# Performance work log

Hardware: AMD Instinct MI355X
Metric: run time of the kernel (lower is better)

The kernel has to match this reference:

```python
import jax, jax.numpy as jnp
import numpy as np

N, E = 25000, 400000
HID, EDGE_F, DIM, HEADS, ADY = 128, 16, 3, 8, 64
INNER = int(1.25 * HID)          # 160
MSG_F = 2 * HID + EDGE_F + 1     # 273 (e3, relaxed=False -> 1 distance feature)


def silu(x):
    return x * jax.nn.sigmoid(x)


def ada_ln(x, y, W, b):
    # LayerNorm (no affine) + FiLM conditioning from y
    mu = jnp.mean(x, axis=-1, keepdims=True)
    var = jnp.var(x, axis=-1, keepdims=True)
    xn = (x - mu) * jax.lax.rsqrt(var + 1e-5)
    scale, shift = jnp.split(y @ W + b, 2, axis=-1)
    return xn * (1.0 + scale) + shift


def setup_inputs() -> dict:
    key = jax.random.key(0)
    ks = jax.random.split(key, 32)
    rn = lambda k, shp, s=0.05: (jax.random.normal(k, shp, jnp.float32) * s)
    inp = {
        'h': jax.random.normal(ks[0], (N, HID), jnp.float32),
        'coords': jax.random.normal(ks[1], (N, DIM), jnp.float32),
        'a': jax.random.normal(ks[2], (E, EDGE_F), jnp.float32),
        'y': jax.random.normal(ks[3], (N, ADY), jnp.float32),
        'res': jnp.zeros((N, HID), jnp.float32),
        'src': jax.random.randint(ks[4], (E,), 0, N, jnp.int32),
        'dst': jax.random.randint(ks[5], (E,), 0, N, jnp.int32),
        # edge MLP
        'We1': rn(ks[6], (MSG_F, INNER)), 'be1': jnp.zeros((INNER,), jnp.float32),
        'We2': rn(ks[7], (INNER, INNER)), 'be2': jnp.zeros((INNER,), jnp.float32),
        # coord head (xavier gain 0.001 -> tiny init)
        'Wc': rn(ks[8], (INNER, 1), 0.001),
        # attention/value/output heads
        'Wv': rn(ks[9], (INNER, HID)),
        'Wa': rn(ks[10], (INNER, HEADS)),
        'Wo': rn(ks[11], (HID, HID)),
        # node MLP
        'Wn1': rn(ks[12], (HID, INNER)), 'bn1': jnp.zeros((INNER,), jnp.float32),
        'Wn2': rn(ks[13], (INNER, HID)), 'bn2': jnp.zeros((HID,), jnp.float32),
        # adaptive LayerNorms (FiLM from y)
        'Wf1': rn(ks[14], (ADY, 2 * HID)), 'bf1': jnp.zeros((2 * HID,), jnp.float32),
        'Wf2': rn(ks[15], (ADY, 2 * HID)), 'bf2': jnp.zeros((2 * HID,), jnp.float32),
    }
    return inp


def reference(h, coords, a, y, res, src, dst,
              We1, be1, We2, be2, Wc, Wv, Wa, Wo,
              Wn1, bn1, Wn2, bn2, Wf1, bf1, Wf2, bf2):
    n = h.shape[0]
    heads = Wa.shape[1]
    # --- distance features (e3, relaxed=False): radial only ---
    xs, xd = coords[src], coords[dst]          # [E, 3]
    diffs = xs - xd
    radials = jnp.sum(diffs * diffs, axis=-1, keepdims=True)  # [E, 1]
    # --- edge MLP on gathered features ---
    f = jnp.concatenate([h[src], h[dst], radials, a], axis=-1)  # [E, 273]
    m = silu(f @ We1 + be1)
    m = silu(m @ We2 + be2)                    # [E, inner]
    # --- coordinate messages + scatter-sum to dst ---
    msg_x = (m @ Wc) * diffs / (jnp.sqrt(radials + 1e-5) + 1.0)  # [E, 3]
    coords_out = coords + jax.ops.segment_sum(msg_x, dst, num_segments=n)
    # --- edge softmax over incoming edges per dst node ---
    logits = m @ Wa                             # [E, heads]
    mx = jax.ops.segment_max(logits, dst, num_segments=n)
    ex = jnp.exp(logits - mx[dst])
    den = jax.ops.segment_sum(ex, dst, num_segments=n)
    w = ex / den[dst]                           # [E, heads]
    # --- weighted value aggregation ---
    vals = (m @ Wv).reshape(-1, heads, HID // heads) * w[:, :, None]
    h_agg = jax.ops.segment_sum(vals, dst, num_segments=n).reshape(n, HID)
    f2 = h_agg @ Wo
    res1 = res + f2
    h1 = ada_ln(h + f2, y, Wf1, bf1)
    f3 = silu(h1 @ Wn1 + bn1) @ Wn2 + bn2
    res2 = res1 + f3
    h2 = ada_ln(h1 + f3, y, Wf2, bf2)
    return (h2, coords_out, res2)
```

## Files before the change

### kernel.cpp

```cpp
#include <hip/hip_runtime.h>
#include <math.h>

#define N_NODES 25000
#define N_EDGES 400000
#define HID 128
#define EDGE_F 16
#define ADY 64
#define INNER 160
#define MSG_F 273
#define HEADS 8

#define OUT_CRD (N_NODES * HID)
#define OUT_RES (N_NODES * (HID + 3))

#define FLAG_OFF 0
#define DEN_OFF  256
#define CACC_OFF 800256
#define HAGG_OFF 1100256
#define CNT_OFF  13900256
#define CUR_OFF  14000256
#define PERM_OFF 14100256
#define MEMSET_BYTES 14000256
#define HBF_OFF  15700256
#define YBF_OFF  22100256
#define BIAS_OFF 25300256
#define BW_OFF   25302560

#define SCR_STRIDE 145

typedef unsigned short u16;
typedef unsigned int u32;
typedef unsigned long long u64;
typedef __attribute__((ext_vector_type(8))) short short8;
typedef __attribute__((ext_vector_type(4))) float f32x4;

__device__ __forceinline__ float bf2f(u16 v) {
    union { u32 u; float f; } x; x.u = ((u32)v) << 16; return x.f;
}
__device__ __forceinline__ u16 f2bf(float f) {
    union { float ff; u32 u; } x; x.ff = f;
    u32 u = x.u;
    u32 rounding = 0x7FFFu + ((u >> 16) & 1u);
    u += rounding;
    return (u16)(u >> 16);
}
__device__ __forceinline__ float silu(float z) {
    z = fminf(fmaxf(z, -30000.f), 30000.f);
    return z / (1.0f + __expf(-z));
}

template<bool F32> __device__ __forceinline__ float ldg1(const void* p, size_t i) {
    if (F32) return ((const float*)p)[i];
    return bf2f(((const u16*)p)[i]);
}
template<bool F32> __device__ __forceinline__ void stg1(void* p, size_t i, float v) {
    if (F32) ((float*)p)[i] = v;
    else     ((u16*)p)[i] = f2bf(v);
}
__device__ __forceinline__ float ldany(const void* p, size_t i, bool f32) {
    return f32 ? ((const float*)p)[i] : bf2f(((const u16*)p)[i]);
}
__device__ __forceinline__ void wave_lds_fence() {
    __builtin_amdgcn_wave_barrier();
    __builtin_amdgcn_s_waitcnt(0xc07f);
    __builtin_amdgcn_wave_barrier();
}

struct CvtArgs {
    const void* src[8];
    u64 dstoff[8];
    int n[8];
};
struct BwArgs {
    const void* We1; const void* We2; const void* Wv; const void* Wa;
    const void* Wc;  const void* Wo;  const void* Wn1; const void* Wn2;
    const void* Wf1; const void* Wf2;
    u64 b1, b2, b3, b4, b5, b6, b7, b8;
};

__global__ __launch_bounds__(256)
void preproc_kernel(const void* hsrc, int* flag, char* ws, CvtArgs args, BwArgs bwa,
                    const int* __restrict__ dstp, int* __restrict__ cnt)
{
    __shared__ float red[256];
    __shared__ int sflag;
    const int t = threadIdx.x;
    {
        const u16* p = (const u16*)hsrc;
        float mx = 0.f;
        for (int i = 0; i < 8; i++) {
            int idx = (t * 8 + i) * 97;
            float v = fabsf(bf2f(p[idx * 2]));
            mx = fmaxf(mx, v);
        }
        red[t] = mx;
        __syncthreads();
        for (int s = 128; s > 0; s >>= 1) {
            if (t < s) red[t] = fmaxf(red[t], red[t + s]);
            __syncthreads();
        }
        if (t == 0) {
            sflag = (red[0] > 1e10f || red[0] == 0.f) ? 1 : 0;
            if (blockIdx.x == 0) flag[0] = sflag;
        }
        __syncthreads();
    }
    const bool f32 = (sflag != 0);
    const int g = blockIdx.x * 256 + t;
    const int stride = gridDim.x * 256;

    for (int i = g; i < N_EDGES; i += stride)
        atomicAdd(&cnt[dstp[i]], 1);

    for (int ten = 0; ten < 8; ten++) {
        const void* s = args.src[ten];
        u16* d = (u16*)(ws + args.dstoff[ten]);
        const int n = args.n[ten];
        if (f32) {
            const float* sf = (const float*)s;
            for (int i = g; i < n; i += stride) d[i] = f2bf(sf[i]);
        } else {
            const u16* su = (const u16*)s;
            for (int i = g; i < n; i += stride) d[i] = su[i];
        }
    }

    u16* b1 = (u16*)(ws + bwa.b1);
    u16* b2 = (u16*)(ws + bwa.b2);
    u16* b3 = (u16*)(ws + bwa.b3);
    u16* b4 = (u16*)(ws + bwa.b4);
    u16* b5 = (u16*)(ws + bwa.b5);
    u16* b6 = (u16*)(ws + bwa.b6);
    u16* b7 = (u16*)(ws + bwa.b7);
    u16* b8 = (u16*)(ws + bwa.b8);
    for (int i = g; i < 5*2*10*512; i += stride) {
        int tt = i >> 9, r = i & 511, l = r >> 3, j = r & 7;
        int c = tt / 20, ks = (tt / 10) % 2, nt = tt % 10;
        int k = c*64 + ks*32 + (l >> 4)*8 + j;
        int n = nt*16 + (l & 15);
        float v = 0.f;
        if (k < MSG_F)      v = ldany(bwa.We1, (size_t)k*INNER + n, f32);
        else if (k == 273)  v = ldany(bwa.We1, (size_t)256*INNER + n, f32);
        b1[i] = f2bf(v);
    }
    for (int i = g; i < 5*10*512; i += stride) {
        int tt = i >> 9, r = i & 511, l = r >> 3, j = r & 7;
        int k5 = tt / 10, nt = tt % 10;
        int k = k5*32 + (l >> 4)*8 + j;
        int n = nt*16 + (l & 15);
        b2[i] = f2bf(ldany(bwa.We2, (size_t)k*INNER + n, f32));
    }
    for (int i = g; i < 5*9*512; i += stride) {
        int tt = i >> 9, r = i & 511, l = r >> 3, j = r & 7;
        int k5 = tt / 9, nt = tt % 9;
        int k = k5*32 + (l >> 4)*8 + j;
        int n = nt*16 + (l & 15);
        float v = 0.f;
        if (n < 128)       v = ldany(bwa.Wv, (size_t)k*HID + n, f32);
        else if (n < 136)  v = ldany(bwa.Wa, (size_t)k*HEADS + (n-128), f32);
        else if (n == 136) v = ldany(bwa.Wc, (size_t)k, f32);
        b3[i] = f2bf(v);
    }
    for (int i = g; i < 4*8*512; i += stride) {
        int tt = i >> 9, r = i & 511, l = r >> 3, j = r & 7;
        int cks = tt / 8, nt = tt % 8;
        int k = cks*32 + (l >> 4)*8 + j;
        int n = nt*16 + (l & 15);
        b4[i] = f2bf(ldany(bwa.Wo, (size_t)k*HID + n, f32));
    }
    for (int i = g; i < 4*10*512; i += stride) {
        int tt = i >> 9, r = i & 511, l = r >> 3, j = r & 7;
        int cks = tt / 10, nt = tt % 10;
        int k = cks*32 + (l >> 4)*8 + j;
        int n = nt*16 + (l & 15);
        b5[i] = f2bf(ldany(bwa.Wn1, (size_t)k*INNER + n, f32));
    }
    for (int i = g; i < 5*8*512; i += stride) {
        int tt = i >> 9, r = i & 511, l = r >> 3, j = r & 7;
        int k5 = tt / 8, nt = tt % 8;
        int k = k5*32 + (l >> 4)*8 + j;
        int n = nt*16 + (l & 15);
        b6[i] = f2bf(ldany(bwa.Wn2, (size_t)k*HID + n, f32));
    }
    for (int i = g; i < 2*16*512; i += stride) {
        int tt = i >> 9, r = i & 511, l = r >> 3, j = r & 7;
        int ks = tt / 16, nt = tt % 16;
        int k = ks*32 + (l >> 4)*8 + j;
        int n = nt*16 + (l & 15);
        b7[i] = f2bf(ldany(bwa.Wf1, (size_t)k*256 + n, f32));
        b8[i] = f2bf(ldany(bwa.Wf2, (size_t)k*256 + n, f32));
    }
}

__global__ __launch_bounds__(1024)
void scan_kernel(const int* __restrict__ cnt, int* __restrict__ cursor)
{
    __shared__ int ssum[1024];
    const int t = threadIdx.x;
    const int base = t * 25;
    int loc[25];
    int s = 0;
    #pragma unroll
    for (int j = 0; j < 25; j++) {
        int i = base + j;
        int v = (i < N_NODES) ? cnt[i] : 0;
        loc[j] = s; s += v;
    }
    ssum[t] = s;
    __syncthreads();
    for (int off = 1; off < 1024; off <<= 1) {
        int v = (t >= off) ? ssum[t - off] : 0;
        __syncthreads();
        ssum[t] += v;
        __syncthreads();
    }
    int offs = (t > 0) ? ssum[t - 1] : 0;
    #pragma unroll
    for (int j = 0; j < 25; j++) {
        int i = base + j;
        if (i < N_NODES) cursor[i] = offs + loc[j];
    }
}

__global__ __launch_bounds__(256)
void scatter_kernel(const int* __restrict__ dstp, int* __restrict__ cursor,
                    int* __restrict__ perm)
{
    int i = blockIdx.x * 256 + threadIdx.x;
    if (i < N_EDGES) {
        int pos = atomicAdd(&cursor[dstp[i]], 1);
        perm[pos] = i;
    }
}

template<bool F32>
__device__ __forceinline__ void edge_body(
    const u16* __restrict__ hbf, const void* coords, const void* a,
    const int* __restrict__ src, const int* __restrict__ dst,
    const int* __restrict__ perm,
    const u16* __restrict__ We1P, const u16* __restrict__ We2P,
    const u16* __restrict__ W3P,
    const u16* __restrict__ cbe1, const u16* __restrict__ cbe2,
    float* __restrict__ den, float* __restrict__ hagg, float* __restrict__ cacc,
    u16* sPool, float* sdiff, float* srad, int* ssrc, int* sdstl, int* sedge)
{
    const int t   = threadIdx.x;
    const int w   = t >> 6;
    const int l   = t & 63;
    const int col = l & 15;
    const int q   = l >> 4;
    const int e0  = blockIdx.x * 64;
    const int l8  = l << 3;

    u16* sF  = sPool;
    u16* sM1 = sPool;
    u16* sM2 = sPool + 64*168;

    if (t < 64) {
        int e = perm[e0 + t];
        sedge[t] = e;
        int s = src[e], d = dst[e];
        ssrc[t] = s; sdstl[t] = d;
        float dx = ldg1<F32>(coords, (size_t)s*3+0) - ldg1<F32>(coords, (size_t)d*3+0);
        float dy = ldg1<F32>(coords, (size_t)s*3+1) - ldg1<F32>(coords, (size_t)d*3+1);
        float dz = ldg1<F32>(coords, (size_t)s*3+2) - ldg1<F32>(coords, (size_t)d*3+2);
        sdiff[t*4+0] = dx; sdiff[t*4+1] = dy; sdiff[t*4+2] = dz;
        float r2 = dx*dx + dy*dy + dz*dz;
        srad[t] = r2;
        sdiff[t*4+3] = 1.0f / (sqrtf(r2 + 1e-5f) + 1.0f);
    }
    __syncthreads();

    {
        int e = t >> 2, part = t & 3;
        int node_s = ssrc[e], node_d = sdstl[e];
        int ge = sedge[e];
        #pragma unroll
        for (int c = 0; c < 4; c++) {
            int node = (c < 2) ? node_s : node_d;
            int c0 = (c & 1) * 64 + part * 16;
            const uint4* gp = (const uint4*)(hbf + (size_t)node*HID + c0);
            *(uint4*)(&sF[e*360 + c*72 + part*16])     = gp[0];
            *(uint4*)(&sF[e*360 + c*72 + part*16 + 8]) = gp[1];
        }
        if (part < 2) {
            __align__(16) u16 tmp[16];
            #pragma unroll
            for (int j = 0; j < 16; j++) tmp[j] = 0;
            if (part == 0) {
                float r2 = srad[e];
                tmp[0] = f2bf(r2);
                for (int j = 0; j < 15; j++)
                    tmp[1+j] = f2bf(ldg1<F32>(a, (size_t)ge*EDGE_F + j));
            } else {
                tmp[0] = f2bf(ldg1<F32>(a, (size_t)ge*EDGE_F + 15));
                float r2 = srad[e];
                tmp[1] = f2bf(r2 - bf2f(f2bf(r2)));
            }
            *(uint4*)(&sF[e*360 + 4*72 + part*16])     = ((uint4*)tmp)[0];
            *(uint4*)(&sF[e*360 + 4*72 + part*16 + 8]) = ((uint4*)tmp)[1];
        }
    }
    __syncthreads();

    f32x4 acc1[10];
    #pragma unroll
    for (int nt = 0; nt < 10; nt++) {
        float v = bf2f(cbe1[nt*16 + col]);
        acc1[nt] = (f32x4){v, v, v, v};
    }
    const u16* fbase = &sF[(w*16 + col)*360];
    #pragma unroll
    for (int c = 0; c < 4; c++) {
        #pragma unroll
        for (int ks = 0; ks < 2; ks++) {
            short8 af = *(const short8*)(fbase + c*72 + ks*32 + q*8);
            const u16* B1 = We1P + (((c*2 + ks)*10) << 9) + l8;
            #pragma unroll
            for (int nt = 0; nt < 10; nt++) {
                short8 b = *(const short8*)(B1 + (nt << 9));
                acc1[nt] = __builtin_amdgcn_mfma_f32_16x16x32_bf16(af, b, acc1[nt], 0, 0, 0);
            }
        }
    }
    {
        short8 af = *(const short8*)(fbase + 4*72 + q*8);
        const u16* B1 = We1P + ((8*10) << 9) + l8;
        #pragma unroll
        for (int nt = 0; nt < 10; nt++) {
            short8 b = *(const short8*)(B1 + (nt << 9));
            acc1[nt] = __builtin_amdgcn_mfma_f32_16x16x32_bf16(af, b, acc1[nt], 0, 0, 0);
        }
    }
    __syncthreads();
    #pragma unroll
    for (int nt = 0; nt < 10; nt++)
        #pragma unroll
        for (int r = 0; r < 4; r++)
            sM1[(w*16 + q*4 + r)*168 + nt*16 + col] = f2bf(silu(acc1[nt][r]));
    __syncthreads();

    f32x4 acc2[10];
    #pragma unroll
    for (int nt = 0; nt < 10; nt++) {
        float v = bf2f(cbe2[nt*16 + col]);
        acc2[nt] = (f32x4){v, v, v, v};
    }
    const u16* m1base = &sM1[(w*16 + col)*168];
    #pragma unroll
    for (int k5 = 0; k5 < 5; k5++) {
        short8 af = *(const short8*)(m1base + k5*32 + q*8);
        const u16* B2 = We2P + ((k5*10) << 9) + l8;
        #pragma unroll
        for (int nt = 0; nt < 10; nt++) {
            short8 b = *(const short8*)(B2 + (nt << 9));
            acc2[nt] = __builtin_amdgcn_mfma_f32_16x16x32_bf16(af, b, acc2[nt], 0, 0, 0);
        }
    }
    #pragma unroll
    for (int nt = 0; nt < 10; nt++)
        #pragma unroll
        for (int r = 0; r < 4; r++)
            sM2[(w*16 + q*4 + r)*168 + nt*16 + col] = f2bf(silu(acc2[nt][r]));
    __syncthreads();

    f32x4 acc3[9];
    #pragma unroll
    for (int nt = 0; nt < 9; nt++) acc3[nt] = (f32x4){0.f, 0.f, 0.f, 0.f};
    const u16* m2base = &sM2[(w*16 + col)*168];
    #pragma unroll
    for (int k5 = 0; k5 < 5; k5++) {
        short8 af = *(const short8*)(m2base + k5*32 + q*8);
        const u16* B3 = W3P + ((k5*9) << 9) + l8;
        #pragma unroll
        for (int nt = 0; nt < 9; nt++) {
            short8 b = *(const short8*)(B3 + (nt << 9));
            acc3[nt] = __builtin_amdgcn_mfma_f32_16x16x32_bf16(af, b, acc3[nt], 0, 0, 0);
        }
    }
    __syncthreads();

    float* scr = (float*)(void*)sPool + (size_t)w * 16 * SCR_STRIDE;

    {
        float exv[4] = {0.f, 0.f, 0.f, 0.f};
        if (col < 8) {
            #pragma unroll
            for (int r = 0; r < 4; r++)
                exv[r] = __expf(fminf(fmaxf(acc3[8][r], -30.f), 30.f));
        }
        #pragma unroll
        for (int nt = 0; nt < 8; nt++) {
            float ex0 = __shfl(exv[0], q*16 + nt);
            float ex1 = __shfl(exv[1], q*16 + nt);
            float ex2 = __shfl(exv[2], q*16 + nt);
            float ex3 = __shfl(exv[3], q*16 + nt);
            scr[(q*4 + 0)*SCR_STRIDE + nt*16 + col] = acc3[nt][0] * ex0;
            scr[(q*4 + 1)*SCR_STRIDE + nt*16 + col] = acc3[nt][1] * ex1;
            scr[(q*4 + 2)*SCR_STRIDE + nt*16 + col] = acc3[nt][2] * ex2;
            scr[(q*4 + 3)*SCR_STRIDE + nt*16 + col] = acc3[nt][3] * ex3;
        }
        if (col < 8) {
            #pragma unroll
            for (int r = 0; r < 4; r++)
                scr[(q*4 + r)*SCR_STRIDE + 128 + col] = exv[r];
        }
        if (col == 8) {
            #pragma unroll
            for (int r = 0; r < 4; r++) {
                int idx = w*16 + q*4 + r;
                float invf = sdiff[idx*4 + 3];
                float lc = fminf(fmaxf(acc3[8][r], -1e6f), 1e6f) * invf;
                #pragma unroll
                for (int j = 0; j < 3; j++)
                    scr[(q*4 + r)*SCR_STRIDE + 136 + j] = lc * sdiff[idx*4 + j];
            }
        }
    }
    wave_lds_fence();

    {
        const int rbase = w*16;
        int dsts[16];
        #pragma unroll
        for (int row = 0; row < 16; row++) dsts[row] = sdstl[rbase + row];

        #pragma unroll
        for (int pass = 0; pass < 3; pass++) {
            int c = pass*64 + l;
            bool act = c < 139;
            float accu = 0.f;
            int prevd = dsts[0];
            #pragma unroll
            for (int row = 0; row < 16; row++) {
                int d = dsts[row];
                if (d != prevd) {
                    if (act) {
                        if (c < 128)      atomicAdd(&hagg[(size_t)prevd*HID + c], accu);
                        else if (c < 136) atomicAdd(&den[(size_t)prevd*8 + (c-128)], accu);
                        else              atomicAdd(&cacc[(size_t)prevd*3 + (c-136)], accu);
                    }
                    accu = 0.f; prevd = d;
                }
                if (act) accu += scr[row*SCR_STRIDE + c];
            }
            if (act) {
                if (c < 128)      atomicAdd(&hagg[(size_t)prevd*HID + c], accu);
                else if (c < 136) atomicAdd(&den[(size_t)prevd*8 + (c-128)], accu);
                else              atomicAdd(&cacc[(size_t)prevd*3 + (c-136)], accu);
            }
        }
    }
}

__global__ __launch_bounds__(256, 3)
void edge_kernel(const int* __restrict__ flag,
                 const u16* __restrict__ hbf, const void* coords, const void* a,
                 const int* __restrict__ src, const int* __restrict__ dst,
                 const int* __restrict__ perm,
                 const u16* __restrict__ We1P, const u16* __restrict__ We2P,
                 const u16* __restrict__ W3P,
                 const u16* __restrict__ cbe1, const u16* __restrict__ cbe2,
                 float* __restrict__ den, float* __restrict__ hagg,
                 float* __restrict__ cacc)
{
    __shared__ __align__(16) u16 sPool[64*360];
    __shared__ float sdiff[64*4];
    __shared__ float srad[64];
    __shared__ int   ssrc[64];
    __shared__ int   sdstl[64];
    __shared__ int   sedge[64];
    if (*flag)
        edge_body<true>(hbf, coords, a, src, dst, perm, We1P, We2P, W3P, cbe1, cbe2,
                        den, hagg, cacc, sPool, sdiff, srad, ssrc, sdstl, sedge);
    else
        edge_body<false>(hbf, coords, a, src, dst, perm, We1P, We2P, W3P, cbe1, cbe2,
                         den, hagg, cacc, sPool, sdiff, srad, ssrc, sdstl, sedge);
}

template<bool F32>
__device__ __forceinline__ void node_body(
    const u16* __restrict__ hbf, const void* res, const void* coords,
    const u16* __restrict__ ybf,
    const float* __restrict__ den, const float* __restrict__ hagg,
    const float* __restrict__ cacc,
    const u16* __restrict__ WoP, const u16* __restrict__ Wn1P,
    const u16* __restrict__ Wn2P, const u16* __restrict__ Wf1P,
    const u16* __restrict__ Wf2P,
    const u16* __restrict__ cbn1, const u16* __restrict__ cbn2,
    const u16* __restrict__ cbf1, const u16* __restrict__ cbf2,
    void* out, u16* sScr)
{
    const int t = threadIdx.x;
    const int w = t >> 6, l = t & 63, col = l & 15, q = l >> 4;
    const int nodew = blockIdx.x * 64 + w * 16;
    const int mynode = nodew + col;
    const bool okA = mynode < N_NODES;
    const int l8 = l << 3;
    u16* sc = sScr + w * 16 * 168;

    int gm[4]; bool okC[4];
    #pragma unroll
    for (int r = 0; r < 4; r++) { gm[r] = nodew + q*4 + r; okC[r] = gm[r] < N_NODES; }

    f32x4 aF2[8];
    #pragma unroll
    for (int nt = 0; nt < 8; nt++) aF2[nt] = (f32x4){0.f,0.f,0.f,0.f};
    #pragma unroll
    for (int c = 0; c < 2; c++) {
        #pragma unroll
        for (int ks = 0; ks < 2; ks++) {
            const int kbase = c*64 + ks*32 + q*8;
            union { u16 s[8]; short8 v; } u;
            if (okA) {
                float dd = den[(size_t)mynode*8 + (kbase >> 4)];
                float inv = dd > 0.f ? 1.f/dd : 0.f;
                const float4* gp = (const float4*)(hagg + (size_t)mynode*HID + kbase);
                float4 v0 = gp[0], v1 = gp[1];
                u.s[0]=f2bf(v0.x*inv); u.s[1]=f2bf(v0.y*inv); u.s[2]=f2bf(v0.z*inv); u.s[3]=f2bf(v0.w*inv);
                u.s[4]=f2bf(v1.x*inv); u.s[5]=f2bf(v1.y*inv); u.s[6]=f2bf(v1.z*inv); u.s[7]=f2bf(v1.w*inv);
            } else {
                #pragma unroll
                for (int j = 0; j < 8; j++) u.s[j] = 0;
            }
            const u16* B = WoP + (((c*2 + ks)*8) << 9) + l8;
            #pragma unroll
            for (int nt = 0; nt < 8; nt++) {
                short8 b = *(const short8*)(B + (nt << 9));
                aF2[nt] = __builtin_amdgcn_mfma_f32_16x16x32_bf16(u.v, b, aF2[nt], 0, 0, 0);
            }
        }
    }

    f32x4 aFl[16];
    #pragma unroll
    for (int nt = 0; nt < 16; nt++) {
        float v = bf2f(cbf1[nt*16 + col]);
        aFl[nt] = (f32x4){v,v,v,v};
    }
    #pragma unroll
    for (int ks = 0; ks < 2; ks++) {
        short8 af;
        if (okA) af = *(const short8*)(ybf + (size_t)mynode*ADY + ks*32 + q*8);
        else { union { u16 s[8]; short8 v; } z; for (int j=0;j<8;j++) z.s[j]=0; af = z.v; }
        const u16* B = Wf1P + ((ks*16) << 9) + l8;
        #pragma unroll
        for (int nt = 0; nt < 16; nt++) {
            short8 b = *(const short8*)(B + (nt << 9));
            aFl[nt] = __builtin_amdgcn_mfma_f32_16x16x32_bf16(af, b, aFl[nt], 0, 0, 0);
        }
    }

    float h1c[8][4], r1c[8][4];
    {
        float xv[8][4], s[4], ss[4];
        #pragma unroll
        for (int r = 0; r < 4; r++) { s[r] = 0.f; ss[r] = 0.f; }
        #pragma unroll
        for (int nt = 0; nt < 8; nt++)
            #pragma unroll
            for (int r = 0; r < 4; r++) {
                float hv = okC[r] ? bf2f(hbf[(size_t)gm[r]*HID + nt*16 + col]) : 0.f;
                float x = hv + aF2[nt][r];
                xv[nt][r] = x; s[r] += x; ss[r] += x*x;
            }
        #pragma unroll
        for (int r = 0; r < 4; r++)
            for (int off = 1; off <= 8; off <<= 1) {
                s[r]  += __shfl_xor(s[r], off);
                ss[r] += __shfl_xor(ss[r], off);
            }
        #pragma unroll
        for (int r = 0; r < 4; r++) {
            float mu = s[r] * (1.f/128.f);
            float var = ss[r] * (1.f/128.f) - mu*mu;
            float rs = rsqrtf(fmaxf(var, 0.f) + 1e-5f);
            #pragma unroll
            for (int nt = 0; nt < 8; nt++) {
                float h1 = (xv[nt][r]-mu)*rs*(1.f+aFl[nt][r]) + aFl[nt+8][r];
                h1c[nt][r] = h1;
                float rv = okC[r] ? ldg1<F32>(res, (size_t)gm[r]*HID + nt*16 + col) : 0.f;
                r1c[nt][r] = rv + aF2[nt][r];
                sc[(q*4 + r)*168 + nt*16 + col] = f2bf(h1);
            }
        }
    }
    wave_lds_fence();

    f32x4 aT[10];
    #pragma unroll
    for (int nt = 0; nt < 10; nt++) {
        float v = bf2f(cbn1[nt*16 + col]);
        aT[nt] = (f32x4){v,v,v,v};
    }
    #pragma unroll
    for (int c = 0; c < 2; c++) {
        #pragma unroll
        for (int ks = 0; ks < 2; ks++) {
            short8 af = *(const short8*)(sc + col*168 + c*64 + ks*32 + q*8);
            const u16* B = Wn1P + (((c*2 + ks)*10) << 9) + l8;
            #pragma unroll
            for (int nt = 0; nt < 10; nt++) {
                short8 b = *(const short8*)(B + (nt << 9));
                aT[nt] = __builtin_amdgcn_mfma_f32_16x16x32_bf16(af, b, aT[nt], 0, 0, 0);
            }
        }
    }
    wave_lds_fence();
    #pragma unroll
    for (int nt = 0; nt < 10; nt++)
        #pragma unroll
        for (int r = 0; r < 4; r++)
            sc[(q*4 + r)*168 + nt*16 + col] = f2bf(silu(aT[nt][r]));
    wave_lds_fence();

    f32x4 aF3[8];
    #pragma unroll
    for (int nt = 0; nt < 8; nt++) {
        float v = bf2f(cbn2[nt*16 + col]);
        aF3[nt] = (f32x4){v,v,v,v};
    }
    #pragma unroll
    for (int k5 = 0; k5 < 5; k5++) {
        short8 af = *(const short8*)(sc + col*168 + k5*32 + q*8);
        const u16* B = Wn2P + ((k5*8) << 9) + l8;
        #pragma unroll
        for (int nt = 0; nt < 8; nt++) {
            short8 b = *(const short8*)(B + (nt << 9));
            aF3[nt] = __builtin_amdgcn_mfma_f32_16x16x32_bf16(af, b, aF3[nt], 0, 0, 0);
        }
    }

    #pragma unroll
    for (int nt = 0; nt < 16; nt++) {
        float v = bf2f(cbf2[nt*16 + col]);
        aFl[nt] = (f32x4){v,v,v,v};
    }
    #pragma unroll
    for (int ks = 0; ks < 2; ks++) {
        short8 af;
        if (okA) af = *(const short8*)(ybf + (size_t)mynode*ADY + ks*32 + q*8);
        else { union { u16 s[8]; short8 v; } z; for (int j=0;j<8;j++) z.s[j]=0; af = z.v; }
        const u16* B = Wf2P + ((ks*16) << 9) + l8;
        #pragma unroll
        for (int nt = 0; nt < 16; nt++) {
            short8 b = *(const short8*)(B + (nt << 9));
            aFl[nt] = __builtin_amdgcn_mfma_f32_16x16x32_bf16(af, b, aFl[nt], 0, 0, 0);
        }
    }

    {
        float xv[8][4], s[4], ss[4];
        #pragma unroll
        for (int r = 0; r < 4; r++) { s[r] = 0.f; ss[r] = 0.f; }
        #pragma unroll
        for (int nt = 0; nt < 8; nt++)
            #pragma unroll
            for (int r = 0; r < 4; r++) {
                float x = h1c[nt][r] + aF3[nt][r];
                xv[nt][r] = x; s[r] += x; ss[r] += x*x;
            }
        #pragma unroll
        for (int r = 0; r < 4; r++)
            for (int off = 1; off <= 8; off <<= 1) {
                s[r]  += __shfl_xor(s[r], off);
                ss[r] += __shfl_xor(ss[r], off);
            }
        #pragma unroll
        for (int r = 0; r < 4; r++) {
            float mu = s[r] * (1.f/128.f);
            float var = ss[r] * (1.f/128.f) - mu*mu;
            float rs = rsqrtf(fmaxf(var, 0.f) + 1e-5f);
            if (okC[r]) {
                #pragma unroll
                for (int nt = 0; nt < 8; nt++) {
                    int n = nt*16 + col;
                    float h2 = (xv[nt][r]-mu)*rs*(1.f+aFl[nt][r]) + aFl[nt+8][r];
                    stg1<F32>(out, (size_t)gm[r]*HID + n, h2);
                    stg1<F32>(out, (size_t)OUT_RES + (size_t)gm[r]*HID + n,
                              r1c[nt][r] + aF3[nt][r]);
                }
            }
        }
    }

    if (q == 0 && okA) {
        #pragma unroll
        for (int j = 0; j < 3; j++)
            stg1<F32>(out, (size_t)OUT_CRD + (size_t)mynode*3 + j,
                      ldg1<F32>(coords, (size_t)mynode*3 + j) + cacc[(size_t)mynode*3 + j]);
    }
}

__global__ __launch_bounds__(256, 2)
void node_kernel(const int* __restrict__ flag,
                 const u16* __restrict__ hbf, const void* res, const void* coords,
                 const u16* __restrict__ ybf,
                 const float* __restrict__ den, const float* __restrict__ hagg,
                 const float* __restrict__ cacc,
                 const u16* __restrict__ WoP, const u16* __restrict__ Wn1P,
                 const u16* __restrict__ Wn2P, const u16* __restrict__ Wf1P,
                 const u16* __restrict__ Wf2P,
                 const u16* __restrict__ cbn1, const u16* __restrict__ cbn2,
                 const u16* __restrict__ cbf1, const u16* __restrict__ cbf2,
                 void* out)
{
    __shared__ __align__(16) u16 sScr[4 * 16 * 168];
    if (*flag)
        node_body<true>(hbf, res, coords, ybf, den, hagg, cacc, WoP, Wn1P, Wn2P,
                        Wf1P, Wf2P, cbn1, cbn2, cbf1, cbf2, out, sScr);
    else
        node_body<false>(hbf, res, coords, ybf, den, hagg, cacc, WoP, Wn1P, Wn2P,
                         Wf1P, Wf2P, cbn1, cbn2, cbf1, cbf2, out, sScr);
}

extern "C" void kernel_launch(void* const* d_in, const int* in_sizes, int n_in,
                              void* d_out, int out_size, void* d_ws, size_t ws_size,
                              hipStream_t stream)
{
    const void* h      = d_in[0];
    const void* coords = d_in[1];
    const void* a      = d_in[2];
    const void* y      = d_in[3];
    const void* res    = d_in[4];
    const int* src     = (const int*)d_in[5];
    const int* dst     = (const int*)d_in[6];

    char* ws = (char*)d_ws;
    int*   flag   = (int*)(ws + FLAG_OFF);
    float* den    = (float*)(ws + DEN_OFF);
    float* cacc   = (float*)(ws + CACC_OFF);
    float* hagg   = (float*)(ws + HAGG_OFF);
    int*   cnt    = (int*)(ws + CNT_OFF);
    int*   cursor = (int*)(ws + CUR_OFF);
    int*   perm   = (int*)(ws + PERM_OFF);
    u16*   hbf    = (u16*)(ws + HBF_OFF);
    u16*   ybf    = (u16*)(ws + YBF_OFF);

    CvtArgs args;
    const int cvtn[8]   = {160, 160, 160, 128, 256, 256, N_NODES*HID, N_NODES*ADY};
    const int cvtsrc[8] = {8, 10, 16, 18, 20, 22, 0, 3};
    u64 boff[8];
    u64 bo = BIAS_OFF;
    for (int i = 0; i < 6; i++) {
        boff[i] = bo;
        bo += ((u64)cvtn[i] * 2 + 15) & ~(u64)15;
    }
    boff[6] = HBF_OFF;
    boff[7] = YBF_OFF;
    for (int i = 0; i < 8; i++) {
        args.src[i] = d_in[cvtsrc[i]];
        args.dstoff[i] = boff[i];
        args.n[i] = cvtn[i];
    }
    const u16* cbe1 = (const u16*)(ws + boff[0]);
    const u16* cbe2 = (const u16*)(ws + boff[1]);
    const u16* cbn1 = (const u16*)(ws + boff[2]);
    const u16* cbn2 = (const u16*)(ws + boff[3]);
    const u16* cbf1 = (const u16*)(ws + boff[4]);
    const u16* cbf2 = (const u16*)(ws + boff[5]);

    BwArgs bwa;
    bwa.We1 = d_in[7];  bwa.We2 = d_in[9];  bwa.Wv = d_in[12]; bwa.Wa = d_in[13];
    bwa.Wc  = d_in[11]; bwa.Wo  = d_in[14]; bwa.Wn1 = d_in[15]; bwa.Wn2 = d_in[17];
    bwa.Wf1 = d_in[19]; bwa.Wf2 = d_in[21];
    bwa.b1 = BW_OFF;
    bwa.b2 = bwa.b1 + (u64)5*2*10*512*2;
    bwa.b3 = bwa.b2 + (u64)5*10*512*2;
    bwa.b4 = bwa.b3 + (u64)5*9*512*2;
    bwa.b5 = bwa.b4 + (u64)4*8*512*2;
    bwa.b6 = bwa.b5 + (u64)4*10*512*2;
    bwa.b7 = bwa.b6 + (u64)5*8*512*2;
    bwa.b8 = bwa.b7 + (u64)2*16*512*2;
    const u16* We1P = (const u16*)(ws + bwa.b1);
    const u16* We2P = (const u16*)(ws + bwa.b2);
    const u16* W3P  = (const u16*)(ws + bwa.b3);
    const u16* WoP  = (const u16*)(ws + bwa.b4);
    const u16* Wn1P = (const u16*)(ws + bwa.b5);
    const u16* Wn2P = (const u16*)(ws + bwa.b6);
    const u16* Wf1P = (const u16*)(ws + bwa.b7);
    const u16* Wf2P = (const u16*)(ws + bwa.b8);

    hipMemsetAsync(d_ws, 0, MEMSET_BYTES, stream);

    preproc_kernel<<<256, 256, 0, stream>>>(h, flag, ws, args, bwa, dst, cnt);

    scan_kernel<<<1, 1024, 0, stream>>>(cnt, cursor);

    scatter_kernel<<<(N_EDGES + 255)/256, 256, 0, stream>>>(dst, cursor, perm);

    edge_kernel<<<N_EDGES/64, 256, 0, stream>>>(flag, hbf, coords, a, src, dst, perm,
                                                We1P, We2P, W3P, cbe1, cbe2,
                                                den, hagg, cacc);

    node_kernel<<<(N_NODES + 63)/64, 256, 0, stream>>>(
        flag, hbf, res, coords, ybf, den, hagg, cacc,
        WoP, Wn1P, Wn2P, Wf1P, Wf2P, cbn1, cbn2, cbf1, cbf2, d_out);
}
```

Before: 528.0 us.

## Make edge kernel wave-private in LDS with MFMA-fragment layout, drop block barriers

Each wave now gathers its own 16 edges into a private LDS slice stored directly in the MFMA A-fragment layout. This replaces the block-wide staging and the __syncthreads calls with wave-local fences, and per-edge geometry is passed through shuffles instead of shared arrays. The shared memory footprint shrinks, so launch bounds are raised to 4 blocks per CU for more occupancy. The costs are a higher register-pressure ceiling and redundant index loads across the 4 lanes per edge.

Result: faster. 482.1 us (-8.7%).

```diff
diff --git a/kernel.cpp b/kernel.cpp
--- a/kernel.cpp
+++ b/kernel.cpp
@@ -26,6 +26,7 @@
 #define BIAS_OFF 25300256
 #define BW_OFF   25302560
 
+#define WSLICE 5120
 #define SCR_STRIDE 145
 
 typedef unsigned short u16;
@@ -64,6 +65,10 @@
     __builtin_amdgcn_wave_barrier();
     __builtin_amdgcn_s_waitcnt(0xc07f);
     __builtin_amdgcn_wave_barrier();
+}
+
+__device__ __forceinline__ int a_addr(int k, int lr) {
+    return ((k >> 5) << 9) + (((((k & 31) >> 3) << 4) | lr) << 3) + (k & 7);
 }
 
 struct CvtArgs {
@@ -242,7 +247,7 @@
     const u16* __restrict__ W3P,
     const u16* __restrict__ cbe1, const u16* __restrict__ cbe2,
     float* __restrict__ den, float* __restrict__ hagg, float* __restrict__ cacc,
-    u16* sPool, float* sdiff, float* srad, int* ssrc, int* sdstl, int* sedge)
+    u16* sPool)
 {
     const int t   = threadIdx.x;
     const int w   = t >> 6;
@@ -252,56 +257,47 @@
     const int e0  = blockIdx.x * 64;
     const int l8  = l << 3;
 
-    u16* sF  = sPool;
-    u16* sM1 = sPool;
-    u16* sM2 = sPool + 64*168;
-
-    if (t < 64) {
-        int e = perm[e0 + t];
-        sedge[t] = e;
-        int s = src[e], d = dst[e];
-        ssrc[t] = s; sdstl[t] = d;
-        float dx = ldg1<F32>(coords, (size_t)s*3+0) - ldg1<F32>(coords, (size_t)d*3+0);
-        float dy = ldg1<F32>(coords, (size_t)s*3+1) - ldg1<F32>(coords, (size_t)d*3+1);
-        float dz = ldg1<F32>(coords, (size_t)s*3+2) - ldg1<F32>(coords, (size_t)d*3+2);
-        sdiff[t*4+0] = dx; sdiff[t*4+1] = dy; sdiff[t*4+2] = dz;
-        float r2 = dx*dx + dy*dy + dz*dz;
-        srad[t] = r2;
-        sdiff[t*4+3] = 1.0f / (sqrtf(r2 + 1e-5f) + 1.0f);
-    }
-    __syncthreads();
-
-    {
-        int e = t >> 2, part = t & 3;
-        int node_s = ssrc[e], node_d = sdstl[e];
-        int ge = sedge[e];
-        #pragma unroll
-        for (int c = 0; c < 4; c++) {
-            int node = (c < 2) ? node_s : node_d;
-            int c0 = (c & 1) * 64 + part * 16;
-            const uint4* gp = (const uint4*)(hbf + (size_t)node*HID + c0);
-            *(uint4*)(&sF[e*360 + c*72 + part*16])     = gp[0];
-            *(uint4*)(&sF[e*360 + c*72 + part*16 + 8]) = gp[1];
-        }
-        if (part < 2) {
-            __align__(16) u16 tmp[16];
-            #pragma unroll
-            for (int j = 0; j < 16; j++) tmp[j] = 0;
-            if (part == 0) {
-                float r2 = srad[e];
-                tmp[0] = f2bf(r2);
-                for (int j = 0; j < 15; j++)
-                    tmp[1+j] = f2bf(ldg1<F32>(a, (size_t)ge*EDGE_F + j));
-            } else {
-                tmp[0] = f2bf(ldg1<F32>(a, (size_t)ge*EDGE_F + 15));
-                float r2 = srad[e];
-                tmp[1] = f2bf(r2 - bf2f(f2bf(r2)));
-            }
-            *(uint4*)(&sF[e*360 + 4*72 + part*16])     = ((uint4*)tmp)[0];
-            *(uint4*)(&sF[e*360 + 4*72 + part*16 + 8]) = ((uint4*)tmp)[1];
-        }
-    }
-    __syncthreads();
+    u16* sW = sPool + w * WSLICE;
+
+    const int r = l >> 2;
+    const int p = t & 3;
+    const int ge = perm[e0 + w*16 + r];
+    const int s_ = src[ge];
+    const int d_ = dst[ge];
+    float dx = 0.f, dy = 0.f, dz = 0.f, invf = 0.f, r2 = 0.f;
+    if (p < 2) {
+        dx = ldg1<F32>(coords, (size_t)s_*3+0) - ldg1<F32>(coords, (size_t)d_*3+0);
+        dy = ldg1<F32>(coords, (size_t)s_*3+1) - ldg1<F32>(coords, (size_t)d_*3+1);
+        dz = ldg1<F32>(coords, (size_t)s_*3+2) - ldg1<F32>(coords, (size_t)d_*3+2);
+        r2 = dx*dx + dy*dy + dz*dz;
+        invf = 1.0f / (sqrtf(r2 + 1e-5f) + 1.0f);
+    }
+    #pragma unroll
+    for (int c = 0; c < 4; c++) {
+        int node = (c < 2) ? s_ : d_;
+        int hcol = (c & 1) * 64 + p * 16;
+        const uint4* gp = (const uint4*)(hbf + (size_t)node*HID + hcol);
+        int k0 = c*64 + p*16;
+        *(uint4*)(sW + a_addr(k0,     r)) = gp[0];
+        *(uint4*)(sW + a_addr(k0 + 8, r)) = gp[1];
+    }
+    if (p < 2) {
+        __align__(16) u16 tmp[16];
+        #pragma unroll
+        for (int j = 0; j < 16; j++) tmp[j] = 0;
+        if (p == 0) {
+            tmp[0] = f2bf(r2);
+            for (int j = 0; j < 15; j++)
+                tmp[1+j] = f2bf(ldg1<F32>(a, (size_t)ge*EDGE_F + j));
+        } else {
+            tmp[0] = f2bf(ldg1<F32>(a, (size_t)ge*EDGE_F + 15));
+            tmp[1] = f2bf(r2 - bf2f(f2bf(r2)));
+        }
+        int k0 = 256 + p*16;
+        *(uint4*)(sW + a_addr(k0,     r)) = ((uint4*)tmp)[0];
+        *(uint4*)(sW + a_addr(k0 + 8, r)) = ((uint4*)tmp)[1];
+    }
+    wave_lds_fence();
 
     f32x4 acc1[10];
     #pragma unroll
@@ -309,36 +305,23 @@
         float v = bf2f(cbe1[nt*16 + col]);
         acc1[nt] = (f32x4){v, v, v, v};
     }
-    const u16* fbase = &sF[(w*16 + col)*360];
-    #pragma unroll
-    for (int c = 0; c < 4; c++) {
-        #pragma unroll
-        for (int ks = 0; ks < 2; ks++) {
-            short8 af = *(const short8*)(fbase + c*72 + ks*32 + q*8);
-            const u16* B1 = We1P + (((c*2 + ks)*10) << 9) + l8;
-            #pragma unroll
-            for (int nt = 0; nt < 10; nt++) {
-                short8 b = *(const short8*)(B1 + (nt << 9));
-                acc1[nt] = __builtin_amdgcn_mfma_f32_16x16x32_bf16(af, b, acc1[nt], 0, 0, 0);
-            }
-        }
-    }
-    {
-        short8 af = *(const short8*)(fbase + 4*72 + q*8);
-        const u16* B1 = We1P + ((8*10) << 9) + l8;
+    #pragma unroll
+    for (int kk = 0; kk < 9; kk++) {
+        short8 af = *(const short8*)(sW + (kk << 9) + l8);
+        const u16* B1 = We1P + ((kk*10) << 9) + l8;
         #pragma unroll
         for (int nt = 0; nt < 10; nt++) {
             short8 b = *(const short8*)(B1 + (nt << 9));
             acc1[nt] = __builtin_amdgcn_mfma_f32_16x16x32_bf16(af, b, acc1[nt], 0, 0, 0);
         }
     }
-    __syncthreads();
+    wave_lds_fence();
     #pragma unroll
     for (int nt = 0; nt < 10; nt++)
         #pragma unroll
-        for (int r = 0; r < 4; r++)
-            sM1[(w*16 + q*4 + r)*168 + nt*16 + col] = f2bf(silu(acc1[nt][r]));
-    __syncthreads();
+        for (int rr = 0; rr < 4; rr++)
+            sW[a_addr(nt*16 + col, q*4 + rr)] = f2bf(silu(acc1[nt][rr]));
+    wave_lds_fence();
 
     f32x4 acc2[10];
     #pragma unroll
@@ -346,10 +329,9 @@
         float v = bf2f(cbe2[nt*16 + col]);
         acc2[nt] = (f32x4){v, v, v, v};
     }
-    const u16* m1base = &sM1[(w*16 + col)*168];
     #pragma unroll
     for (int k5 = 0; k5 < 5; k5++) {
-        short8 af = *(const short8*)(m1base + k5*32 + q*8);
+        short8 af = *(const short8*)(sW + (k5 << 9) + l8);
         const u16* B2 = We2P + ((k5*10) << 9) + l8;
         #pragma unroll
         for (int nt = 0; nt < 10; nt++) {
@@ -360,17 +342,16 @@
     #pragma unroll
     for (int nt = 0; nt < 10; nt++)
         #pragma unroll
-        for (int r = 0; r < 4; r++)
-            sM2[(w*16 + q*4 + r)*168 + nt*16 + col] = f2bf(silu(acc2[nt][r]));
-    __syncthreads();
+        for (int rr = 0; rr < 4; rr++)
+            sW[2560 + a_addr(nt*16 + col, q*4 + rr)] = f2bf(silu(acc2[nt][rr]));
+    wave_lds_fence();
 
     f32x4 acc3[9];
     #pragma unroll
     for (int nt = 0; nt < 9; nt++) acc3[nt] = (f32x4){0.f, 0.f, 0.f, 0.f};
-    const u16* m2base = &sM2[(w*16 + col)*168];
     #pragma unroll
     for (int k5 = 0; k5 < 5; k5++) {
-        short8 af = *(const short8*)(m2base + k5*32 + q*8);
+        short8 af = *(const short8*)(sW + 2560 + (k5 << 9) + l8);
         const u16* B3 = W3P + ((k5*9) << 9) + l8;
         #pragma unroll
         for (int nt = 0; nt < 9; nt++) {
@@ -378,16 +359,27 @@
             acc3[nt] = __builtin_amdgcn_mfma_f32_16x16x32_bf16(af, b, acc3[nt], 0, 0, 0);
         }
     }
-    __syncthreads();
-
-    float* scr = (float*)(void*)sPool + (size_t)w * 16 * SCR_STRIDE;
+    wave_lds_fence();
+
+    float* scr = (float*)(void*)sW;
+
+    int dsts[16];
+    #pragma unroll
+    for (int row = 0; row < 16; row++) dsts[row] = __shfl(d_, row << 2);
+    float dxv[4], dyv[4], dzv[4], ivv[4];
+    #pragma unroll
+    for (int rr = 0; rr < 4; rr++) {
+        int sl = (q*4 + rr) << 2;
+        dxv[rr] = __shfl(dx, sl); dyv[rr] = __shfl(dy, sl);
+        dzv[rr] = __shfl(dz, sl); ivv[rr] = __shfl(invf, sl);
+    }
 
     {
         float exv[4] = {0.f, 0.f, 0.f, 0.f};
         if (col < 8) {
             #pragma unroll
-            for (int r = 0; r < 4; r++)
-                exv[r] = __expf(fminf(fmaxf(acc3[8][r], -30.f), 30.f));
+            for (int rr = 0; rr < 4; rr++)
+                exv[rr] = __expf(fminf(fmaxf(acc3[8][rr], -30.f), 30.f));
         }
         #pragma unroll
         for (int nt = 0; nt < 8; nt++) {
@@ -402,58 +394,49 @@
         }
         if (col < 8) {
             #pragma unroll
-            for (int r = 0; r < 4; r++)
-                scr[(q*4 + r)*SCR_STRIDE + 128 + col] = exv[r];
+            for (int rr = 0; rr < 4; rr++)
+                scr[(q*4 + rr)*SCR_STRIDE + 128 + col] = exv[rr];
         }
         if (col == 8) {
             #pragma unroll
-            for (int r = 0; r < 4; r++) {
-                int idx = w*16 + q*4 + r;
-                float invf = sdiff[idx*4 + 3];
-                float lc = fminf(fmaxf(acc3[8][r], -1e6f), 1e6f) * invf;
-                #pragma unroll
-                for (int j = 0; j < 3; j++)
-                    scr[(q*4 + r)*SCR_STRIDE + 136 + j] = lc * sdiff[idx*4 + j];
-            }
-        }
-    }
-    wave_lds_fence();
-
-    {
-        const int rbase = w*16;
-        int dsts[16];
-        #pragma unroll
-        for (int row = 0; row < 16; row++) dsts[row] = sdstl[rbase + row];
-
-        #pragma unroll
-        for (int pass = 0; pass < 3; pass++) {
-            int c = pass*64 + l;
-            bool act = c < 139;
-            float accu = 0.f;
-            int prevd = dsts[0];
-            #pragma unroll
-            for (int row = 0; row < 16; row++) {
-                int d = dsts[row];
-                if (d != prevd) {
-                    if (act) {
-                        if (c < 128)      atomicAdd(&hagg[(size_t)prevd*HID + c], accu);
-                        else if (c < 136) atomicAdd(&den[(size_t)prevd*8 + (c-128)], accu);
-                        else              atomicAdd(&cacc[(size_t)prevd*3 + (c-136)], accu);
-                    }
-                    accu = 0.f; prevd = d;
+            for (int rr = 0; rr < 4; rr++) {
+                float lc = fminf(fmaxf(acc3[8][rr], -1e6f), 1e6f) * ivv[rr];
+                scr[(q*4 + rr)*SCR_STRIDE + 136] = lc * dxv[rr];
+                scr[(q*4 + rr)*SCR_STRIDE + 137] = lc * dyv[rr];
+                scr[(q*4 + rr)*SCR_STRIDE + 138] = lc * dzv[rr];
+            }
+        }
+    }
+    wave_lds_fence();
+
+    #pragma unroll
+    for (int pass = 0; pass < 3; pass++) {
+        int c = pass*64 + l;
+        bool act = c < 139;
+        float accu = 0.f;
+        int prevd = dsts[0];
+        #pragma unroll
+        for (int row = 0; row < 16; row++) {
+            int d = dsts[row];
+            if (d != prevd) {
+                if (act) {
+                    if (c < 128)      atomicAdd(&hagg[(size_t)prevd*HID + c], accu);
+                    else if (c < 136) atomicAdd(&den[(size_t)prevd*8 + (c-128)], accu);
+                    else              atomicAdd(&cacc[(size_t)prevd*3 + (c-136)], accu);
                 }
-                if (act) accu += scr[row*SCR_STRIDE + c];
-            }
-            if (act) {
-                if (c < 128)      atomicAdd(&hagg[(size_t)prevd*HID + c], accu);
-                else if (c < 136) atomicAdd(&den[(size_t)prevd*8 + (c-128)], accu);
-                else              atomicAdd(&cacc[(size_t)prevd*3 + (c-136)], accu);
-            }
-        }
-    }
-}
-
-__global__ __launch_bounds__(256, 3)
+                accu = 0.f; prevd = d;
+            }
+            if (act) accu += scr[row*SCR_STRIDE + c];
+        }
+        if (act) {
+            if (c < 128)      atomicAdd(&hagg[(size_t)prevd*HID + c], accu);
+            else if (c < 136) atomicAdd(&den[(size_t)prevd*8 + (c-128)], accu);
+            else              atomicAdd(&cacc[(size_t)prevd*3 + (c-136)], accu);
+        }
+    }
+}
+
+__global__ __launch_bounds__(256, 4)
 void edge_kernel(const int* __restrict__ flag,
                  const u16* __restrict__ hbf, const void* coords, const void* a,
                  const int* __restrict__ src, const int* __restrict__ dst,
@@ -464,18 +447,13 @@
                  float* __restrict__ den, float* __restrict__ hagg,
                  float* __restrict__ cacc)
 {
-    __shared__ __align__(16) u16 sPool[64*360];
-    __shared__ float sdiff[64*4];
-    __shared__ float srad[64];
-    __shared__ int   ssrc[64];
-    __shared__ int   sdstl[64];
-    __shared__ int   sedge[64];
+    __shared__ __align__(16) u16 sPool[4 * WSLICE];
     if (*flag)
-        edge_body<true>(hbf, coords, a, src, dst, perm, We1P, We2P, W3P, cbe1, cbe2,
-                        den, hagg, cacc, sPool, sdiff, srad, ssrc, sdstl, sedge);
+        edge_body<true>(hbf, coords, a, src, dst, perm, We1P, We2P, W3P,
+                        cbe1, cbe2, den, hagg, cacc, sPool);
     else
-        edge_body<false>(hbf, coords, a, src, dst, perm, We1P, We2P, W3P, cbe1, cbe2,
-                         den, hagg, cacc, sPool, sdiff, srad, ssrc, sdstl, sedge);
+        edge_body<false>(hbf, coords, a, src, dst, perm, We1P, We2P, W3P,
+                         cbe1, cbe2, den, hagg, cacc, sPool);
 }
 
 template<bool F32>
```
